# Kernel tuning notes

Measured on AMD Instinct MI355X. Metric: run time of the kernel, lower is better.

The kernel has to match this reference:

```python
import jax, jax.numpy as jnp
import numpy as np

B, T, D, H = 32, 512, 1024, 1024


def setup_inputs() -> dict:
    key = jax.random.key(0)
    k1, k2, k3 = jax.random.split(key, 3)
    x = jax.random.normal(k1, (B, T, D), dtype=jnp.float32)
    c0 = jnp.zeros((B, H), dtype=jnp.float32)
    h0 = jnp.zeros((B, H), dtype=jnp.float32)
    # scale weights so gates do not saturate
    Wx = jax.random.normal(k2, (D, 4 * H), dtype=jnp.float32) * 0.05
    Wh = jax.random.normal(k3, (H, 4 * H), dtype=jnp.float32) * 0.05
    b = jnp.zeros((4 * H,), dtype=jnp.float32)
    return {"x": x, "c0": c0, "h0": h0, "Wx": Wx, "Wh": Wh, "b": b}


def reference(x, c0, h0, Wx, Wh, b):
    # Flax LSTMCell: gates = x @ Wx + h @ Wh + b, split into i,f,g,o.
    # Precompute the input projection for all timesteps (one big GEMM).
    xW = jnp.einsum('btd,dg->btg', x, Wx) + b  # [B,T,4H]

    def step(carry, xw_t):
        c, h = carry
        gates = xw_t + h @ Wh  # [B,4H]
        i, f, g, o = jnp.split(gates, 4, axis=-1)
        i = jax.nn.sigmoid(i)
        f = jax.nn.sigmoid(f)
        g = jnp.tanh(g)
        o = jax.nn.sigmoid(o)
        c_new = f * c + i * g
        h_new = o * jnp.tanh(c_new)
        return (c_new, h_new), h_new

    (cT, hT), ys = jax.lax.scan(step, (c0, h0), jnp.swapaxes(xW, 0, 1))
    outputs = jnp.swapaxes(ys, 0, 1)  # [B,T,H]
    return outputs, (cT, hT)
```

## Files before the change

### kernel.cpp

```cpp
#include <hip/hip_runtime.h>
#include <cstddef>

#define NB 32
#define NT 512
#define ND 1024
#define NH 1024
#define NG 4096
#define GRID 256

typedef unsigned short ushortT;
typedef __attribute__((ext_vector_type(8))) short short8;
typedef __attribute__((ext_vector_type(4))) float f32x4;
typedef __attribute__((ext_vector_type(4))) unsigned uint4v;

#define GLL16(g, l) __builtin_amdgcn_global_load_lds(                      \
    (const __attribute__((address_space(1))) void*)(g),                    \
    (__attribute__((address_space(3))) void*)(l), 16, 0, 0)

__device__ __forceinline__ ushortT f2bf(float f) {
    union { float f; unsigned u; } v; v.f = f;
    unsigned r = v.u + 0x7FFFu + ((v.u >> 16) & 1u);
    return (ushortT)(r >> 16);
}
__device__ __forceinline__ float bf2f(ushortT u) {
    union { unsigned u; float f; } v; v.u = (unsigned)u << 16; return v.f;
}

__device__ __forceinline__ float pick4(float a0, float a1, float a2, float a3, int s) {
    float lo = (s & 1) ? a1 : a0;
    float hi = (s & 1) ? a3 : a2;
    return (s & 2) ? hi : lo;
}

__device__ __forceinline__ float fsigmoid(float x) {
    return __builtin_amdgcn_rcpf(1.f + __expf(-x));
}
__device__ __forceinline__ float ftanh(float x) {
    float xc = fminf(fmaxf(x, -15.f), 15.f);
    float e  = __expf(-2.f * xc);
    return (1.f - e) * __builtin_amdgcn_rcpf(1.f + e);
}

__global__ __launch_bounds__(256) void cast_bf16(const float* __restrict__ src,
                                                 ushortT* __restrict__ dst, int n4)
{
    int i = blockIdx.x * 256 + threadIdx.x;
    if (i < n4) {
        float4 v = ((const float4*)src)[i];
        ushort4 o;
        o.x = f2bf(v.x); o.y = f2bf(v.y); o.z = f2bf(v.z); o.w = f2bf(v.w);
        ((ushort4*)dst)[i] = o;
    }
}

__global__ __launch_bounds__(256) void transpose_cast(
    const float* __restrict__ src, ushortT* __restrict__ dst, int permute)
{
    __shared__ ushortT tile[64][66];
    const int c0 = blockIdx.x * 64, r0 = blockIdx.y * 64;
    const int cc = threadIdx.x & 63, rq = threadIdx.x >> 6;
    #pragma unroll
    for (int ps = 0; ps < 16; ++ps) {
        int r = ps * 4 + rq;
        tile[cc][r] = f2bf(src[(size_t)(r0 + r) * NG + c0 + cc]);
    }
    __syncthreads();
    #pragma unroll
    for (int ps = 0; ps < 16; ++ps) {
        int cl = ps * 4 + rq;
        int n  = c0 + cl;
        int drow = permute ? ((((n & 1023) >> 2) << 4) | ((n >> 10) << 2) | (n & 3))
                           : n;
        dst[(size_t)drow * 1024 + r0 + cc] = tile[cl][cc];
    }
}

__global__ __launch_bounds__(256) void gemm_xw_mfma(
    const ushortT* __restrict__ xb,
    const ushortT* __restrict__ wxT,
    const float* __restrict__ bias,
    ushortT* __restrict__ XWPb,
    int t0, int Tc, int tcsh)
{
    __shared__ ushortT As[128 * 32];
    __shared__ ushortT Bs[128 * 32];

    const int tid  = threadIdx.x;
    const int lane = tid & 63;
    const int wv   = tid >> 6;
    const int wr   = wv >> 1, wc = wv & 1;
    const int n0   = blockIdx.x * 128;
    const int m0   = blockIdx.y * 128;

    const int c1 = tid, c2 = tid + 256;
    const int rm1 = m0 + (c1 >> 2), rm2 = m0 + (c2 >> 2);
    const int xr1 = ((rm1 >> tcsh) * NT) + t0 + (rm1 & (Tc - 1));
    const int xr2 = ((rm2 >> tcsh) * NT) + t0 + (rm2 & (Tc - 1));
    const ushortT* ap1 = xb + (size_t)xr1 * ND + (c1 & 3) * 8;
    const ushortT* ap2 = xb + (size_t)xr2 * ND + (c2 & 3) * 8;
    const ushortT* bp1 = wxT + (size_t)(n0 + (c1 >> 2)) * ND + (c1 & 3) * 8;
    const ushortT* bp2 = wxT + (size_t)(n0 + (c2 >> 2)) * ND + (c2 & 3) * 8;

    f32x4 acc[4][4];
    #pragma unroll
    for (int m = 0; m < 4; ++m)
        #pragma unroll
        for (int n = 0; n < 4; ++n) acc[m][n] = (f32x4){0.f, 0.f, 0.f, 0.f};

    const int arow_base = (wr * 64 + (lane & 15)) * 32 + (lane >> 4) * 8;
    const int brow_base = (wc * 64 + (lane & 15)) * 32 + (lane >> 4) * 8;

    for (int k0 = 0; k0 < ND; k0 += 32) {
        __syncthreads();
        GLL16(ap1 + k0, &As[c1 * 8]);
        GLL16(ap2 + k0, &As[c2 * 8]);
        GLL16(bp1 + k0, &Bs[c1 * 8]);
        GLL16(bp2 + k0, &Bs[c2 * 8]);
        __syncthreads();
        short8 af[4], bf[4];
        #pragma unroll
        for (int m = 0; m < 4; ++m)
            af[m] = *(const short8*)&As[arow_base + m * 16 * 32];
        #pragma unroll
        for (int n = 0; n < 4; ++n)
            bf[n] = *(const short8*)&Bs[brow_base + n * 16 * 32];
        #pragma unroll
        for (int m = 0; m < 4; ++m)
            #pragma unroll
            for (int n = 0; n < 4; ++n)
                acc[m][n] = __builtin_amdgcn_mfma_f32_16x16x32_bf16(
                    af[m], bf[n], acc[m][n], 0, 0, 0);
    }

    #pragma unroll
    for (int n = 0; n < 4; ++n) {
        int col = n0 + wc * 64 + n * 16 + (lane & 15);
        int pc  = (((col & 1023) >> 2) << 4) | ((col >> 10) << 2) | (col & 3);
        float bs = bias[col];
        #pragma unroll
        for (int m = 0; m < 4; ++m) {
            #pragma unroll
            for (int r = 0; r < 4; ++r) {
                int rm = m0 + wr * 64 + m * 16 + (lane >> 4) * 4 + r;
                int b  = rm >> tcsh, tr = rm & (Tc - 1);
                XWPb[((size_t)tr * NB + b) * NG + pc] = f2bf(acc[m][n][r] + bs);
            }
        }
    }
}

__global__ __launch_bounds__(512) void lstm_persist(
    const ushortT* __restrict__ XWPb,
    const ushortT* __restrict__ whpT,
    unsigned* __restrict__ hb0,
    unsigned* __restrict__ hb1,
    const float* __restrict__ cinit,
    float* __restrict__ cT,
    float* __restrict__ out,
    float* __restrict__ hT,
    unsigned* __restrict__ flags,
    int t0, int Tc)
{
    __shared__ ushortT hs[8 * 2048];
    __shared__ float  red[16 * 272];

    const int tid  = threadIdx.x;
    const int lane = tid & 63;
    const int wv   = tid >> 6;
    const int grp  = blockIdx.x & 1;
    const int s    = blockIdx.x >> 1;

    const int lo = lane & 15;
    const int hi = lane >> 4;

    const int rrow  = tid >> 5;
    const int col32 = tid & 31;
    const int rct   = col32 >> 4, rc16 = col32 & 15;
    const int gq    = (col32 >> 2) & 3;
    const int uu    = (col32 >> 4) * 4 + (col32 & 3);
    const int j     = s * 8 + uu;
    const int brow  = grp * 16 + rrow;

    short8 Bf[2][4];
    #pragma unroll
    for (int ct = 0; ct < 2; ++ct)
        #pragma unroll
        for (int ks = 0; ks < 4; ++ks)
            Bf[ct][ks] = *(const short8*)(whpT
                + (size_t)(s * 32 + ct * 16 + lo) * NH + wv * 128 + ks * 32 + hi * 8);

    float creg = cinit[(size_t)brow * NH + j];

    unsigned* const gf = flags + grp * 1024;
    const unsigned long long* fp =
        (const unsigned long long*)(gf + 128 * wv + 2 * lane);

    ushortT xvr = XWPb[(size_t)brow * NG + s * 32 + col32];

    const int tend = t0 + Tc;
    for (int t = t0; t < tend; ++t) {
        const int trel = t - t0;
        const unsigned* hR = ((t & 1) ? hb0 : hb1) + grp * 8192;
        unsigned*       hW = ((t & 1) ? hb1 : hb0) + grp * 8192;

        if (trel) {
            const unsigned tgt = (unsigned)trel;
            int it = 0;
            for (;;) {
                unsigned long long v = __hip_atomic_load(
                    fp, __ATOMIC_RELAXED, __HIP_MEMORY_SCOPE_AGENT);
                bool ok = ((unsigned)v >= tgt) && ((unsigned)(v >> 32) >= tgt);
                if (__all(ok) || ++it > (1 << 16)) break;
            }
        }

        #pragma unroll
        for (int u = 0; u < 4; ++u) {
            int cc  = lane + u * 64;
            int row = cc >> 4, seg = cc & 15;
            const unsigned long long* sp =
                (const unsigned long long*)(hR + row * 512 + wv * 64 + seg * 4);
            unsigned long long v0 = __hip_atomic_load(sp,     __ATOMIC_RELAXED,
                                                      __HIP_MEMORY_SCOPE_AGENT);
            unsigned long long v1 = __hip_atomic_load(sp + 1, __ATOMIC_RELAXED,
                                                      __HIP_MEMORY_SCOPE_AGENT);
            unsigned byte = (unsigned)(wv * 4096 + row * 256)
                          + (((unsigned)seg * 16u) ^ (((unsigned)(row & 7)) << 4));
            *(uint4v*)((char*)hs + byte) =
                (uint4v){(unsigned)v0, (unsigned)(v0 >> 32),
                         (unsigned)v1, (unsigned)(v1 >> 32)};
        }
        float xv = bf2f(xvr);

        f32x4 acc0 = (f32x4){0.f, 0.f, 0.f, 0.f};
        f32x4 acc1 = (f32x4){0.f, 0.f, 0.f, 0.f};
        #pragma unroll
        for (int ks = 0; ks < 4; ++ks) {
            unsigned ab = (unsigned)(wv * 4096 + lo * 256)
                        + (((unsigned)(ks * 64 + hi * 16)) ^ (((unsigned)(lo & 7)) << 4));
            short8 a = *(const short8*)((char*)hs + ab);
            acc0 = __builtin_amdgcn_mfma_f32_16x16x32_bf16(a, Bf[0][ks], acc0, 0, 0, 0);
            acc1 = __builtin_amdgcn_mfma_f32_16x16x32_bf16(a, Bf[1][ks], acc1, 0, 0, 0);
        }
        #pragma unroll
        for (int r = 0; r < 4; ++r) {
            red[(wv * 2 + 0) * 272 + (hi * 4 + r) * 17 + lo] = acc0[r];
            red[(wv * 2 + 1) * 272 + (hi * 4 + r) * 17 + lo] = acc1[r];
        }
        __syncthreads();

        float g = xv;
        #pragma unroll
        for (int w = 0; w < 8; ++w)
            g += red[(w * 2 + rct) * 272 + rrow * 17 + rc16];
        __syncthreads();

        float g4  = __shfl_xor(g, 4);
        float g8  = __shfl_xor(g, 8);
        float g12 = __shfl_xor(g, 12);

        float gi = pick4(g, g4, g8, g12, gq);
        float gf_ = pick4(g, g4, g8, g12, gq ^ 1);
        float gg = pick4(g, g4, g8, g12, gq ^ 2);
        float go = pick4(g, g4, g8, g12, gq ^ 3);

        float iv = fsigmoid(gi);
        float fv = fsigmoid(gf_);
        float gv = ftanh(gg);
        float ov = fsigmoid(go);
        float cn = fv * creg + iv * gv;
        float hn = ov * ftanh(cn);
        creg = cn;

        float ph = __shfl_xor(hn, 1);
        const bool wl = (gq == 0) && ((col32 & 1) == 0);
        if (wl) {
            unsigned pair = (unsigned)f2bf(hn) | ((unsigned)f2bf(ph) << 16);
            __hip_atomic_store(&hW[rrow * 512 + (j >> 1)], pair,
                               __ATOMIC_RELAXED, __HIP_MEMORY_SCOPE_AGENT);
        }

        if (t != tend - 1) {
            asm volatile("s_waitcnt vmcnt(0)" ::: "memory");
            if (lane == 0)
                __hip_atomic_store(&gf[s * 8 + wv], (unsigned)(trel + 1),
                                   __ATOMIC_RELAXED, __HIP_MEMORY_SCOPE_AGENT);
            if (wl)
                *(float2*)&out[((size_t)brow * NT + t) * NH + j] = make_float2(hn, ph);
            xvr = XWPb[((size_t)(trel + 1) * NB + brow) * NG + s * 32 + col32];
        } else {
            if (wl)
                *(float2*)&out[((size_t)brow * NT + t) * NH + j] = make_float2(hn, ph);
            if (gq == 0) {
                if (t == NT - 1) hT[(size_t)brow * NH + j] = hn;
                cT[(size_t)brow * NH + j] = cn;
            }
        }
    }
}

extern "C" void kernel_launch(void* const* d_in, const int* in_sizes, int n_in,
                              void* d_out, int out_size, void* d_ws, size_t ws_size,
                              hipStream_t stream) {
    const float* x    = (const float*)d_in[0];
    const float* c0   = (const float*)d_in[1];
    const float* h0   = (const float*)d_in[2];
    const float* Wx   = (const float*)d_in[3];
    const float* Wh   = (const float*)d_in[4];
    const float* bias = (const float*)d_in[5];

    float* out = (float*)d_out;
    float* cT  = out + (size_t)NB * NT * NH;
    float* hT  = cT + (size_t)NB * NH;

    ushortT* xb   = (ushortT*)d_ws;
    ushortT* wxT  = xb  + (size_t)NB * NT * ND;
    ushortT* whpT = wxT + (size_t)NG * ND;
    unsigned* hb0 = (unsigned*)(whpT + (size_t)NG * NH);
    unsigned* hb1 = hb0 + NB * NH / 2;
    unsigned* flags = hb1 + NB * NH / 2;
    ushortT* xwpb = (ushortT*)(flags + 2 * 1024);

    const size_t fixed = ((size_t)NB * NT * ND + (size_t)NG * ND + (size_t)NG * NH
                          + 2 * NB * NH) * sizeof(ushortT) + 2 * 1024 * 4 + 256;
    int Tc = 512;
    while (Tc > 4 && fixed + (size_t)NB * Tc * NG * sizeof(ushortT) > ws_size)
        Tc >>= 1;
    int tcsh = 31 - __builtin_clz(Tc);

    cast_bf16<<<(NB * NT * ND / 4 + 255) / 256, 256, 0, stream>>>(x, xb, NB * NT * ND / 4);
    cast_bf16<<<(NB * NH / 4 + 255) / 256, 256, 0, stream>>>(h0, (ushortT*)hb1, NB * NH / 4);
    transpose_cast<<<dim3(64, 16), 256, 0, stream>>>(Wx, wxT, 0);
    transpose_cast<<<dim3(64, 16), 256, 0, stream>>>(Wh, whpT, 1);

    for (int t0 = 0; t0 < NT; t0 += Tc) {
        dim3 g(NG / 128, (NB * Tc) / 128);
        gemm_xw_mfma<<<g, 256, 0, stream>>>(xb, wxT, bias, xwpb, t0, Tc, tcsh);
        hipMemsetAsync(flags, 0, 2 * 1024 * sizeof(unsigned), stream);
        lstm_persist<<<GRID, 512, 0, stream>>>(
            xwpb, whpT, hb0, hb1,
            (t0 == 0) ? c0 : (const float*)cT,
            cT, out, hT, flags, t0, Tc);
    }
}
```

Measured before the change: 2.057 ms.

## Repartition persistent LSTM into 8 batch groups with register-resident A fragments

The recurrent kernel now splits work into 8 batch groups of 4 rows and 32 column slices of 128 gate columns, instead of 2 groups of 16 rows and 128 slices of 32 columns. Each wave holds 8 column tiles of Wh in registers and loads h fragments straight from global memory into MFMA registers, skipping the LDS staging. Each group waits on only 32 flags rather than 1024, with one flag per block written after a block barrier. The intent is to cut synchronisation fan-in and LDS traffic per timestep. In exchange it uses many more registers for B fragments and computes MFMAs on padded 16-row tiles where only 4 rows are valid.

```diff
diff --git a/kernel.cpp b/kernel.cpp
--- a/kernel.cpp
+++ b/kernel.cpp
@@ -152,8 +152,7 @@
 __global__ __launch_bounds__(512) void lstm_persist(
     const ushortT* __restrict__ XWPb,
     const ushortT* __restrict__ whpT,
-    unsigned* __restrict__ hb0,
-    unsigned* __restrict__ hb1,
+    ushortT* __restrict__ hbuf,
     const float* __restrict__ cinit,
     float* __restrict__ cT,
     float* __restrict__ out,
@@ -161,111 +160,107 @@
     unsigned* __restrict__ flags,
     int t0, int Tc)
 {
-    __shared__ ushortT hs[8 * 2048];
-    __shared__ float  red[16 * 272];
+    __shared__ float red[2][64][16][4];
 
     const int tid  = threadIdx.x;
     const int lane = tid & 63;
-    const int wv   = tid >> 6;
-    const int grp  = blockIdx.x & 1;
-    const int s    = blockIdx.x >> 1;
+    const int w    = tid >> 6;
+    const int grp  = blockIdx.x & 7;
+    const int sl   = blockIdx.x >> 3;
 
     const int lo = lane & 15;
     const int hi = lane >> 4;
 
-    const int rrow  = tid >> 5;
-    const int col32 = tid & 31;
-    const int rct   = col32 >> 4, rc16 = col32 & 15;
-    const int gq    = (col32 >> 2) & 3;
-    const int uu    = (col32 >> 4) * 4 + (col32 & 3);
-    const int j     = s * 8 + uu;
-    const int brow  = grp * 16 + rrow;
-
-    short8 Bf[2][4];
-    #pragma unroll
-    for (int ct = 0; ct < 2; ++ct)
+    short8 Bf[8][4];
+    #pragma unroll
+    for (int ct = 0; ct < 8; ++ct)
         #pragma unroll
         for (int ks = 0; ks < 4; ++ks)
             Bf[ct][ks] = *(const short8*)(whpT
-                + (size_t)(s * 32 + ct * 16 + lo) * NH + wv * 128 + ks * 32 + hi * 8);
+                + (size_t)(sl * 128 + ct * 16 + lo) * NH + w * 128 + ks * 32 + hi * 8);
+
+    const int arow = tid >> 7;
+    const int acol = tid & 127;
+    const int gq   = (acol >> 2) & 3;
+    const int u4   = (acol >> 4) * 4 + (acol & 3);
+    const int brow = grp * 4 + arow;
+    const int j    = sl * 32 + u4;
 
     float creg = cinit[(size_t)brow * NH + j];
 
-    unsigned* const gf = flags + grp * 1024;
-    const unsigned long long* fp =
-        (const unsigned long long*)(gf + 128 * wv + 2 * lane);
-
-    ushortT xvr = XWPb[(size_t)brow * NG + s * 32 + col32];
+    const int aoff = (grp * 4 + (lane & 3)) * NH + w * 128 + hi * 8;
+
+    unsigned* const fg = flags + grp * 32;
+    unsigned* const fpoll = fg + 4 * w + (lane & 3);
+    unsigned* const fmine = fg + sl;
+
+    ushortT xvr = XWPb[(size_t)brow * NG + sl * 128 + acol];
 
     const int tend = t0 + Tc;
     for (int t = t0; t < tend; ++t) {
         const int trel = t - t0;
-        const unsigned* hR = ((t & 1) ? hb0 : hb1) + grp * 8192;
-        unsigned*       hW = ((t & 1) ? hb1 : hb0) + grp * 8192;
+        const int par  = t & 1;
+        const ushortT* hRp = hbuf + (size_t)par * (NB * NH);
+        ushortT*       hWp = hbuf + (size_t)(par ^ 1) * (NB * NH);
 
         if (trel) {
             const unsigned tgt = (unsigned)trel;
-            int it = 0;
-            for (;;) {
-                unsigned long long v = __hip_atomic_load(
-                    fp, __ATOMIC_RELAXED, __HIP_MEMORY_SCOPE_AGENT);
-                bool ok = ((unsigned)v >= tgt) && ((unsigned)(v >> 32) >= tgt);
-                if (__all(ok) || ++it > (1 << 16)) break;
+            for (int it = 0; it < (1 << 17); ++it) {
+                unsigned v = __hip_atomic_load(fpoll, __ATOMIC_RELAXED,
+                                               __HIP_MEMORY_SCOPE_AGENT);
+                if (__all(v >= tgt)) break;
             }
         }
 
-        #pragma unroll
-        for (int u = 0; u < 4; ++u) {
-            int cc  = lane + u * 64;
-            int row = cc >> 4, seg = cc & 15;
-            const unsigned long long* sp =
-                (const unsigned long long*)(hR + row * 512 + wv * 64 + seg * 4);
-            unsigned long long v0 = __hip_atomic_load(sp,     __ATOMIC_RELAXED,
-                                                      __HIP_MEMORY_SCOPE_AGENT);
-            unsigned long long v1 = __hip_atomic_load(sp + 1, __ATOMIC_RELAXED,
-                                                      __HIP_MEMORY_SCOPE_AGENT);
-            unsigned byte = (unsigned)(wv * 4096 + row * 256)
-                          + (((unsigned)seg * 16u) ^ (((unsigned)(row & 7)) << 4));
-            *(uint4v*)((char*)hs + byte) =
-                (uint4v){(unsigned)v0, (unsigned)(v0 >> 32),
-                         (unsigned)v1, (unsigned)(v1 >> 32)};
-        }
-        float xv = bf2f(xvr);
-
-        f32x4 acc0 = (f32x4){0.f, 0.f, 0.f, 0.f};
-        f32x4 acc1 = (f32x4){0.f, 0.f, 0.f, 0.f};
-        #pragma unroll
-        for (int ks = 0; ks < 4; ++ks) {
-            unsigned ab = (unsigned)(wv * 4096 + lo * 256)
-                        + (((unsigned)(ks * 64 + hi * 16)) ^ (((unsigned)(lo & 7)) << 4));
-            short8 a = *(const short8*)((char*)hs + ab);
-            acc0 = __builtin_amdgcn_mfma_f32_16x16x32_bf16(a, Bf[0][ks], acc0, 0, 0, 0);
-            acc1 = __builtin_amdgcn_mfma_f32_16x16x32_bf16(a, Bf[1][ks], acc1, 0, 0, 0);
-        }
-        #pragma unroll
-        for (int r = 0; r < 4; ++r) {
-            red[(wv * 2 + 0) * 272 + (hi * 4 + r) * 17 + lo] = acc0[r];
-            red[(wv * 2 + 1) * 272 + (hi * 4 + r) * 17 + lo] = acc1[r];
+        const unsigned long long* sp = (const unsigned long long*)(hRp + aoff);
+        unsigned long long p0, p1;
+        uint4v Araw0, Araw1, Araw2, Araw3;
+        p0 = __hip_atomic_load(sp + 0, __ATOMIC_RELAXED, __HIP_MEMORY_SCOPE_AGENT);
+        p1 = __hip_atomic_load(sp + 1, __ATOMIC_RELAXED, __HIP_MEMORY_SCOPE_AGENT);
+        Araw0 = (uint4v){(unsigned)p0, (unsigned)(p0 >> 32), (unsigned)p1, (unsigned)(p1 >> 32)};
+        p0 = __hip_atomic_load(sp + 8, __ATOMIC_RELAXED, __HIP_MEMORY_SCOPE_AGENT);
+        p1 = __hip_atomic_load(sp + 9, __ATOMIC_RELAXED, __HIP_MEMORY_SCOPE_AGENT);
+        Araw1 = (uint4v){(unsigned)p0, (unsigned)(p0 >> 32), (unsigned)p1, (unsigned)(p1 >> 32)};
+        p0 = __hip_atomic_load(sp + 16, __ATOMIC_RELAXED, __HIP_MEMORY_SCOPE_AGENT);
+        p1 = __hip_atomic_load(sp + 17, __ATOMIC_RELAXED, __HIP_MEMORY_SCOPE_AGENT);
+        Araw2 = (uint4v){(unsigned)p0, (unsigned)(p0 >> 32), (unsigned)p1, (unsigned)(p1 >> 32)};
+        p0 = __hip_atomic_load(sp + 24, __ATOMIC_RELAXED, __HIP_MEMORY_SCOPE_AGENT);
+        p1 = __hip_atomic_load(sp + 25, __ATOMIC_RELAXED, __HIP_MEMORY_SCOPE_AGENT);
+        Araw3 = (uint4v){(unsigned)p0, (unsigned)(p0 >> 32), (unsigned)p1, (unsigned)(p1 >> 32)};
+
+        short8 A0 = *(short8*)&Araw0;
+        short8 A1 = *(short8*)&Araw1;
+        short8 A2 = *(short8*)&Araw2;
+        short8 A3 = *(short8*)&Araw3;
+
+        #pragma unroll
+        for (int ct = 0; ct < 8; ++ct) {
+            f32x4 a = (f32x4){0.f, 0.f, 0.f, 0.f};
+            a = __builtin_amdgcn_mfma_f32_16x16x32_bf16(A0, Bf[ct][0], a, 0, 0, 0);
+            a = __builtin_amdgcn_mfma_f32_16x16x32_bf16(A1, Bf[ct][1], a, 0, 0, 0);
+            a = __builtin_amdgcn_mfma_f32_16x16x32_bf16(A2, Bf[ct][2], a, 0, 0, 0);
+            a = __builtin_amdgcn_mfma_f32_16x16x32_bf16(A3, Bf[ct][3], a, 0, 0, 0);
+            if (hi == 0)
+                *(f32x4*)&red[par][w * 8 + ct][lo][0] = a;
         }
         __syncthreads();
 
-        float g = xv;
-        #pragma unroll
-        for (int w = 0; w < 8; ++w)
-            g += red[(w * 2 + rct) * 272 + rrow * 17 + rc16];
-        __syncthreads();
+        float g = bf2f(xvr);
+        #pragma unroll
+        for (int wv = 0; wv < 8; ++wv)
+            g += red[par][wv * 8 + (acol >> 4)][acol & 15][arow];
 
         float g4  = __shfl_xor(g, 4);
         float g8  = __shfl_xor(g, 8);
         float g12 = __shfl_xor(g, 12);
 
         float gi = pick4(g, g4, g8, g12, gq);
-        float gf_ = pick4(g, g4, g8, g12, gq ^ 1);
+        float gf = pick4(g, g4, g8, g12, gq ^ 1);
         float gg = pick4(g, g4, g8, g12, gq ^ 2);
         float go = pick4(g, g4, g8, g12, gq ^ 3);
 
         float iv = fsigmoid(gi);
-        float fv = fsigmoid(gf_);
+        float fv = fsigmoid(gf);
         float gv = ftanh(gg);
         float ov = fsigmoid(go);
         float cn = fv * creg + iv * gv;
@@ -273,21 +268,23 @@
         creg = cn;
 
         float ph = __shfl_xor(hn, 1);
-        const bool wl = (gq == 0) && ((col32 & 1) == 0);
-        if (wl) {
-            unsigned pair = (unsigned)f2bf(hn) | ((unsigned)f2bf(ph) << 16);
-            __hip_atomic_store(&hW[rrow * 512 + (j >> 1)], pair,
-                               __ATOMIC_RELAXED, __HIP_MEMORY_SCOPE_AGENT);
-        }
+        const bool wl = (gq == 0) && ((acol & 1) == 0);
+        unsigned pair = (unsigned)f2bf(hn) | ((unsigned)f2bf(ph) << 16);
+        unsigned* hdst = (unsigned*)(hWp + (size_t)brow * NH + (j & ~1));
+        if (wl)
+            __hip_atomic_store(hdst, pair, __ATOMIC_RELAXED,
+                               __HIP_MEMORY_SCOPE_AGENT);
+
+        asm volatile("s_waitcnt vmcnt(0)" ::: "memory");
+        __syncthreads();
 
         if (t != tend - 1) {
-            asm volatile("s_waitcnt vmcnt(0)" ::: "memory");
-            if (lane == 0)
-                __hip_atomic_store(&gf[s * 8 + wv], (unsigned)(trel + 1),
+            if (tid == 0)
+                __hip_atomic_store(fmine, (unsigned)(trel + 1),
                                    __ATOMIC_RELAXED, __HIP_MEMORY_SCOPE_AGENT);
             if (wl)
                 *(float2*)&out[((size_t)brow * NT + t) * NH + j] = make_float2(hn, ph);
-            xvr = XWPb[((size_t)(trel + 1) * NB + brow) * NG + s * 32 + col32];
+            xvr = XWPb[((size_t)(trel + 1) * NB + brow) * NG + sl * 128 + acol];
         } else {
             if (wl)
                 *(float2*)&out[((size_t)brow * NT + t) * NH + j] = make_float2(hn, ph);
@@ -316,29 +313,29 @@
     ushortT* xb   = (ushortT*)d_ws;
     ushortT* wxT  = xb  + (size_t)NB * NT * ND;
     ushortT* whpT = wxT + (size_t)NG * ND;
-    unsigned* hb0 = (unsigned*)(whpT + (size_t)NG * NH);
-    unsigned* hb1 = hb0 + NB * NH / 2;
-    unsigned* flags = hb1 + NB * NH / 2;
-    ushortT* xwpb = (ushortT*)(flags + 2 * 1024);
+    ushortT* hbuf = whpT + (size_t)NG * NH;
+    unsigned* flags = (unsigned*)(hbuf + 2 * NB * NH);
+    ushortT* xwpb = (ushortT*)(flags + 8 * 32 + 32);
 
     const size_t fixed = ((size_t)NB * NT * ND + (size_t)NG * ND + (size_t)NG * NH
-                          + 2 * NB * NH) * sizeof(ushortT) + 2 * 1024 * 4 + 256;
+                          + 2 * NB * NH) * sizeof(ushortT)
+                         + (8 * 32 + 32) * sizeof(unsigned) + 256;
     int Tc = 512;
     while (Tc > 4 && fixed + (size_t)NB * Tc * NG * sizeof(ushortT) > ws_size)
         Tc >>= 1;
     int tcsh = 31 - __builtin_clz(Tc);
 
     cast_bf16<<<(NB * NT * ND / 4 + 255) / 256, 256, 0, stream>>>(x, xb, NB * NT * ND / 4);
-    cast_bf16<<<(NB * NH / 4 + 255) / 256, 256, 0, stream>>>(h0, (ushortT*)hb1, NB * NH / 4);
+    cast_bf16<<<(NB * NH / 4 + 255) / 256, 256, 0, stream>>>(h0, hbuf, NB * NH / 4);
     transpose_cast<<<dim3(64, 16), 256, 0, stream>>>(Wx, wxT, 0);
     transpose_cast<<<dim3(64, 16), 256, 0, stream>>>(Wh, whpT, 1);
 
     for (int t0 = 0; t0 < NT; t0 += Tc) {
         dim3 g(NG / 128, (NB * Tc) / 128);
         gemm_xw_mfma<<<g, 256, 0, stream>>>(xb, wxT, bias, xwpb, t0, Tc, tcsh);
-        hipMemsetAsync(flags, 0, 2 * 1024 * sizeof(unsigned), stream);
+        hipMemsetAsync(flags, 0, (8 * 32) * sizeof(unsigned), stream);
         lstm_persist<<<GRID, 512, 0, stream>>>(
-            xwpb, whpT, hb0, hb1,
+            xwpb, whpT, hbuf,
             (t0 == 0) ? c0 : (const float*)cT,
             cT, out, hT, flags, t0, Tc);
     }
```

Result: slower. 2.370 ms (+15.2%).

## Load h directly into MFMA fragments and double-buffer reduction to drop a barrier

Applied to the files above, without the earlier changes.

The recurrent h tile is now loaded from global memory straight into per-lane MFMA A-fragments, so the LDS staging buffer, its swizzled writes and its reads are gone. The cross-wave reduction buffer is double-buffered by timestep parity, which removes the second __syncthreads per step. The spin-wait cap is restructured into a bounded for loop. The cost is less coalesced, more scattered global loads per lane, and the removed barrier relies on the flag handshake to keep the two parities from overlapping.

```diff
diff --git a/kernel.cpp b/kernel.cpp
--- a/kernel.cpp
+++ b/kernel.cpp
@@ -9,6 +9,7 @@
 #define GRID 256
 
 typedef unsigned short ushortT;
+typedef unsigned long long u64;
 typedef __attribute__((ext_vector_type(8))) short short8;
 typedef __attribute__((ext_vector_type(4))) float f32x4;
 typedef __attribute__((ext_vector_type(4))) unsigned uint4v;
@@ -161,12 +162,11 @@
     unsigned* __restrict__ flags,
     int t0, int Tc)
 {
-    __shared__ ushortT hs[8 * 2048];
-    __shared__ float  red[16 * 272];
+    __shared__ float red[2][16 * 272];
 
     const int tid  = threadIdx.x;
     const int lane = tid & 63;
-    const int wv   = tid >> 6;
+    const int w    = tid >> 6;
     const int grp  = blockIdx.x & 1;
     const int s    = blockIdx.x >> 1;
 
@@ -187,85 +187,90 @@
         #pragma unroll
         for (int ks = 0; ks < 4; ++ks)
             Bf[ct][ks] = *(const short8*)(whpT
-                + (size_t)(s * 32 + ct * 16 + lo) * NH + wv * 128 + ks * 32 + hi * 8);
+                + (size_t)(s * 32 + ct * 16 + lo) * NH + w * 128 + ks * 32 + hi * 8);
 
     float creg = cinit[(size_t)brow * NH + j];
 
+    const size_t abase64 = (size_t)lo * 256 + w * 32 + hi * 2;
+
     unsigned* const gf = flags + grp * 1024;
-    const unsigned long long* fp =
-        (const unsigned long long*)(gf + 128 * wv + 2 * lane);
+    const u64* fp = (const u64*)(gf + 128 * w + 2 * lane);
+    unsigned* const fmine = gf + s * 8 + w;
 
     ushortT xvr = XWPb[(size_t)brow * NG + s * 32 + col32];
 
     const int tend = t0 + Tc;
     for (int t = t0; t < tend; ++t) {
         const int trel = t - t0;
+        const int par  = t & 1;
         const unsigned* hR = ((t & 1) ? hb0 : hb1) + grp * 8192;
         unsigned*       hW = ((t & 1) ? hb1 : hb0) + grp * 8192;
 
         if (trel) {
             const unsigned tgt = (unsigned)trel;
-            int it = 0;
-            for (;;) {
-                unsigned long long v = __hip_atomic_load(
-                    fp, __ATOMIC_RELAXED, __HIP_MEMORY_SCOPE_AGENT);
+            for (int it = 0; it < (1 << 17); ++it) {
+                u64 v = __hip_atomic_load(fp, __ATOMIC_RELAXED,
+                                          __HIP_MEMORY_SCOPE_AGENT);
                 bool ok = ((unsigned)v >= tgt) && ((unsigned)(v >> 32) >= tgt);
-                if (__all(ok) || ++it > (1 << 16)) break;
+                if (__all(ok)) break;
             }
         }
 
-        #pragma unroll
-        for (int u = 0; u < 4; ++u) {
-            int cc  = lane + u * 64;
-            int row = cc >> 4, seg = cc & 15;
-            const unsigned long long* sp =
-                (const unsigned long long*)(hR + row * 512 + wv * 64 + seg * 4);
-            unsigned long long v0 = __hip_atomic_load(sp,     __ATOMIC_RELAXED,
-                                                      __HIP_MEMORY_SCOPE_AGENT);
-            unsigned long long v1 = __hip_atomic_load(sp + 1, __ATOMIC_RELAXED,
-                                                      __HIP_MEMORY_SCOPE_AGENT);
-            unsigned byte = (unsigned)(wv * 4096 + row * 256)
-                          + (((unsigned)seg * 16u) ^ (((unsigned)(row & 7)) << 4));
-            *(uint4v*)((char*)hs + byte) =
-                (uint4v){(unsigned)v0, (unsigned)(v0 >> 32),
-                         (unsigned)v1, (unsigned)(v1 >> 32)};
-        }
-        float xv = bf2f(xvr);
+        const u64* ap = (const u64*)hR + abase64;
+        u64 q0, q1;
+        uint4v d0, d1, d2, d3;
+        q0 = __hip_atomic_load(ap + 0,  __ATOMIC_RELAXED, __HIP_MEMORY_SCOPE_AGENT);
+        q1 = __hip_atomic_load(ap + 1,  __ATOMIC_RELAXED, __HIP_MEMORY_SCOPE_AGENT);
+        d0 = (uint4v){(unsigned)q0, (unsigned)(q0 >> 32), (unsigned)q1, (unsigned)(q1 >> 32)};
+        q0 = __hip_atomic_load(ap + 8,  __ATOMIC_RELAXED, __HIP_MEMORY_SCOPE_AGENT);
+        q1 = __hip_atomic_load(ap + 9,  __ATOMIC_RELAXED, __HIP_MEMORY_SCOPE_AGENT);
+        d1 = (uint4v){(unsigned)q0, (unsigned)(q0 >> 32), (unsigned)q1, (unsigned)(q1 >> 32)};
+        q0 = __hip_atomic_load(ap + 16, __ATOMIC_RELAXED, __HIP_MEMORY_SCOPE_AGENT);
+        q1 = __hip_atomic_load(ap + 17, __ATOMIC_RELAXED, __HIP_MEMORY_SCOPE_AGENT);
+        d2 = (uint4v){(unsigned)q0, (unsigned)(q0 >> 32), (unsigned)q1, (unsigned)(q1 >> 32)};
+        q0 = __hip_atomic_load(ap + 24, __ATOMIC_RELAXED, __HIP_MEMORY_SCOPE_AGENT);
+        q1 = __hip_atomic_load(ap + 25, __ATOMIC_RELAXED, __HIP_MEMORY_SCOPE_AGENT);
+        d3 = (uint4v){(unsigned)q0, (unsigned)(q0 >> 32), (unsigned)q1, (unsigned)(q1 >> 32)};
+
+        short8 A0 = *(short8*)&d0;
+        short8 A1 = *(short8*)&d1;
+        short8 A2 = *(short8*)&d2;
+        short8 A3 = *(short8*)&d3;
 
         f32x4 acc0 = (f32x4){0.f, 0.f, 0.f, 0.f};
         f32x4 acc1 = (f32x4){0.f, 0.f, 0.f, 0.f};
-        #pragma unroll
-        for (int ks = 0; ks < 4; ++ks) {
-            unsigned ab = (unsigned)(wv * 4096 + lo * 256)
-                        + (((unsigned)(ks * 64 + hi * 16)) ^ (((unsigned)(lo & 7)) << 4));
-            short8 a = *(const short8*)((char*)hs + ab);
-            acc0 = __builtin_amdgcn_mfma_f32_16x16x32_bf16(a, Bf[0][ks], acc0, 0, 0, 0);
-            acc1 = __builtin_amdgcn_mfma_f32_16x16x32_bf16(a, Bf[1][ks], acc1, 0, 0, 0);
-        }
+        acc0 = __builtin_amdgcn_mfma_f32_16x16x32_bf16(A0, Bf[0][0], acc0, 0, 0, 0);
+        acc1 = __builtin_amdgcn_mfma_f32_16x16x32_bf16(A0, Bf[1][0], acc1, 0, 0, 0);
+        acc0 = __builtin_amdgcn_mfma_f32_16x16x32_bf16(A1, Bf[0][1], acc0, 0, 0, 0);
+        acc1 = __builtin_amdgcn_mfma_f32_16x16x32_bf16(A1, Bf[1][1], acc1, 0, 0, 0);
+        acc0 = __builtin_amdgcn_mfma_f32_16x16x32_bf16(A2, Bf[0][2], acc0, 0, 0, 0);
+        acc1 = __builtin_amdgcn_mfma_f32_16x16x32_bf16(A2, Bf[1][2], acc1, 0, 0, 0);
+        acc0 = __builtin_amdgcn_mfma_f32_16x16x32_bf16(A3, Bf[0][3], acc0, 0, 0, 0);
+        acc1 = __builtin_amdgcn_mfma_f32_16x16x32_bf16(A3, Bf[1][3], acc1, 0, 0, 0);
+
         #pragma unroll
         for (int r = 0; r < 4; ++r) {
-            red[(wv * 2 + 0) * 272 + (hi * 4 + r) * 17 + lo] = acc0[r];
-            red[(wv * 2 + 1) * 272 + (hi * 4 + r) * 17 + lo] = acc1[r];
+            red[par][(w * 2 + 0) * 272 + (hi * 4 + r) * 17 + lo] = acc0[r];
+            red[par][(w * 2 + 1) * 272 + (hi * 4 + r) * 17 + lo] = acc1[r];
         }
         __syncthreads();
 
-        float g = xv;
-        #pragma unroll
-        for (int w = 0; w < 8; ++w)
-            g += red[(w * 2 + rct) * 272 + rrow * 17 + rc16];
-        __syncthreads();
+        float g = bf2f(xvr);
+        #pragma unroll
+        for (int wv = 0; wv < 8; ++wv)
+            g += red[par][(wv * 2 + rct) * 272 + rrow * 17 + rc16];
 
         float g4  = __shfl_xor(g, 4);
         float g8  = __shfl_xor(g, 8);
         float g12 = __shfl_xor(g, 12);
 
         float gi = pick4(g, g4, g8, g12, gq);
-        float gf_ = pick4(g, g4, g8, g12, gq ^ 1);
+        float gf = pick4(g, g4, g8, g12, gq ^ 1);
         float gg = pick4(g, g4, g8, g12, gq ^ 2);
         float go = pick4(g, g4, g8, g12, gq ^ 3);
 
         float iv = fsigmoid(gi);
-        float fv = fsigmoid(gf_);
+        float fv = fsigmoid(gf);
         float gv = ftanh(gg);
         float ov = fsigmoid(go);
         float cn = fv * creg + iv * gv;
@@ -283,7 +288,7 @@
         if (t != tend - 1) {
             asm volatile("s_waitcnt vmcnt(0)" ::: "memory");
             if (lane == 0)
-                __hip_atomic_store(&gf[s * 8 + wv], (unsigned)(trel + 1),
+                __hip_atomic_store(fmine, (unsigned)(trel + 1),
                                    __ATOMIC_RELAXED, __HIP_MEMORY_SCOPE_AGENT);
             if (wl)
                 *(float2*)&out[((size_t)brow * NT + t) * NH + j] = make_float2(hn, ph);
```

Measured after the change: 2.312 ms. 12.4% more time.
